# Kernel optimization log

Measured on AMD Instinct MI355X. Metric: run time of the kernel, lower is better.

The kernel has to match this reference:

```python
import jax, jax.numpy as jnp
import numpy as np

B, SQ, SV = 2, 2048, 2048
DV, DQ, DK, DO, H = 1024, 1280, 1024, 1024, 16
DHK, DHO = DK // H, DO // H


def setup_inputs() -> dict:
    key = jax.random.key(0)
    ks = jax.random.split(key, 8)
    pre_value_key = jax.random.normal(ks[0], (B, SV, DV), jnp.float32)
    pre_query = jax.random.normal(ks[1], (B, SQ, DQ), jnp.float32)
    value_key_masks = (jax.random.uniform(ks[2], (B, SV)) < 0.9).astype(jnp.float32)
    value_key_counts = jnp.maximum(value_key_masks.sum(-1), 1.0)
    s = 0.02
    Wq = jax.random.normal(ks[3], (DQ, DK), jnp.float32) * s
    bq = jnp.zeros((DK,), jnp.float32)
    Wk = jax.random.normal(ks[4], (DV, DK), jnp.float32) * s
    bk = jnp.zeros((DK,), jnp.float32)
    Wv = jax.random.normal(ks[5], (DV, DO), jnp.float32) * s
    bv = jnp.zeros((DO,), jnp.float32)
    overall_gain = jnp.ones((1, H, 1, 1), jnp.float32)
    overall_bias = jnp.full((1, H, 1, 1), -10.0, jnp.float32)
    return dict(pre_value_key=pre_value_key, pre_query=pre_query,
                value_key_masks=value_key_masks, value_key_counts=value_key_counts,
                Wq=Wq, bq=bq, Wk=Wk, bk=bk, Wv=Wv, bv=bv,
                overall_gain=overall_gain, overall_bias=overall_bias)


def _heads(x, h):
    # (B, S, D) -> (B, h, S, D//h)
    b, s, d = x.shape
    return x.reshape(b, s, h, d // h).transpose(0, 2, 1, 3)


def reference(pre_value_key, pre_query, value_key_masks, value_key_counts,
              Wq, bq, Wk, bk, Wv, bv, overall_gain, overall_bias):
    q = _heads(pre_query @ Wq + bq, H)        # (B,H,SQ,DHK)
    k = _heads(pre_value_key @ Wk + bk, H)    # (B,H,SV,DHK)
    v = _heads(pre_value_key @ Wv + bv, H)    # (B,H,SV,DHO)

    scores = jnp.einsum('bhqd,bhkd->bhqk', q, k) / jnp.sqrt(jnp.float32(DHK))

    mask = value_key_masks  # (B,SV), 0/1 float
    # pooled-score sigmoid gate (cross-attn branch)
    pooled = (scores * mask[:, None, None, :]).sum(-1, keepdims=True)
    pooled = pooled / value_key_counts[:, None, None, None]
    overall_weight = jax.nn.sigmoid(pooled * overall_gain + overall_bias)  # (B,H,SQ,1)

    add_mask = jnp.where(mask == 0, -jnp.inf, 0.0).astype(scores.dtype)
    sm = jax.nn.softmax(scores + add_mask[:, None, None, :], axis=-1)
    h = jnp.einsum('bhqk,bhkd->bhqd', sm, v)  # (B,H,SQ,DHO)

    pq_split = _heads(pre_query[:, :, :DO], H)  # (B,H,SQ,DHO)
    out = pq_split * (1.0 - overall_weight) + h * overall_weight
    out = out.transpose(0, 2, 1, 3).reshape(B, SQ, DO)
    out = jnp.concatenate([out, pre_query[:, :, DO:]], axis=-1)  # (B,SQ,DQ)
    return out
```

## Files before the change

kernel.cpp:

```cpp
#include <hip/hip_runtime.h>

typedef __attribute__((ext_vector_type(8))) __bf16 bf16x8;
typedef __attribute__((ext_vector_type(4))) float f32x4;
typedef __attribute__((ext_vector_type(16))) float f32x16;
typedef __attribute__((ext_vector_type(4))) unsigned short us4;
typedef __attribute__((ext_vector_type(4))) unsigned int u32x4;
typedef __attribute__((address_space(3))) void* as3vp;
typedef const __attribute__((address_space(1))) void* as1vp;

#define GLOAD_LDS16(g, l) __builtin_amdgcn_global_load_lds((as1vp)(g), (as3vp)(l), 16, 0, 0)

#if __has_builtin(__builtin_amdgcn_exp2f)
#define EXP2(x) __builtin_amdgcn_exp2f(x)
#else
#define EXP2(x) __expf((x) * 0.6931471805599453f)
#endif

__device__ __forceinline__ unsigned short f2bf(float f) {
  unsigned u = __builtin_bit_cast(unsigned, f);
  u += 0x7FFFu + ((u >> 16) & 1u);
  return (unsigned short)(u >> 16);
}
__device__ __forceinline__ float bf2f(unsigned short u) {
  return __builtin_bit_cast(float, (unsigned)u << 16);
}
__device__ __forceinline__ unsigned int pkbf(float a, float b) {
  unsigned int r;
  asm("v_cvt_pk_bf16_f32 %0, %1, %2" : "=v"(r) : "v"(a), "v"(b));
  return r;
}

__global__ void prep_all(const float* __restrict__ pre_q, const float* __restrict__ pre_vk,
                         const float* __restrict__ Wq, const float* __restrict__ Wk,
                         const float* __restrict__ Wv,
                         unsigned short* __restrict__ pq_bf, unsigned short* __restrict__ pv_bf,
                         unsigned short* __restrict__ WqT, unsigned short* __restrict__ WkT,
                         unsigned short* __restrict__ WvT, float* __restrict__ out) {
  __shared__ float tsh[32][33];
  const int bid = blockIdx.x, tid = threadIdx.x;
  if (bid < 5120) {
    const int i = bid * 256 + tid;
    float4 v = ((const float4*)pre_q)[i];
    us4 o;
    o.x = f2bf(v.x); o.y = f2bf(v.y); o.z = f2bf(v.z); o.w = f2bf(v.w);
    ((us4*)pq_bf)[i] = o;
    if ((i % 320) >= 256) ((float4*)out)[i] = v;
  } else if (bid < 9216) {
    const int i = (bid - 5120) * 256 + tid;
    float4 v = ((const float4*)pre_vk)[i];
    us4 o;
    o.x = f2bf(v.x); o.y = f2bf(v.y); o.z = f2bf(v.z); o.w = f2bf(v.w);
    ((us4*)pv_bf)[i] = o;
  } else {
    const int tb = bid - 9216;
    const int z = tb / 1280, rem = tb % 1280;
    const int x = rem & 31, y = rem >> 5;
    const int K = (z == 0) ? 1280 : 1024;
    if (y * 32 >= K) return;
    const float* W = (z == 0) ? Wq : ((z == 1) ? Wk : Wv);
    unsigned short* WT = (z == 0) ? WqT : ((z == 1) ? WkT : WvT);
    const int tx = tid & 31, ty = tid >> 5;
    const int n0 = x * 32, k0 = y * 32;
#pragma unroll
    for (int i = 0; i < 32; i += 8)
      tsh[ty + i][tx] = W[(size_t)(k0 + ty + i) * 1024 + n0 + tx];
    __syncthreads();
#pragma unroll
    for (int i = 0; i < 32; i += 8)
      WT[(size_t)(n0 + ty + i) * K + k0 + tx] = f2bf(tsh[tx][ty + i]);
  }
}

__global__ void km_reduce(const unsigned short* __restrict__ Kbb, const float* __restrict__ mask,
                          float* __restrict__ km, float* __restrict__ addm) {
  if (blockIdx.x < 16) {
    const int i = blockIdx.x * 256 + threadIdx.x;
    addm[i] = (mask[i] != 0.f) ? 0.f : -1e30f;
  }
  __shared__ float red[16][64];
  const int bh = blockIdx.x >> 3, chunk = blockIdx.x & 7;
  const int b = bh >> 4;
  const int dg = (threadIdx.x & 15) * 4, rg = threadIdx.x >> 4;
  const unsigned short* kb = Kbb + (size_t)(b * 2048) * 1024 + (bh & 15) * 64 + dg;
  const float* mr = mask + b * 2048;
  float a0 = 0.f, a1 = 0.f, a2 = 0.f, a3 = 0.f;
  const int kv0 = chunk * 256;
#pragma unroll 4
  for (int kv = kv0 + rg; kv < kv0 + 256; kv += 16) {
    const float mv = mr[kv];
    us4 kq = *(const us4*)(kb + (size_t)kv * 1024);
    a0 = fmaf(mv, bf2f(kq.x), a0); a1 = fmaf(mv, bf2f(kq.y), a1);
    a2 = fmaf(mv, bf2f(kq.z), a2); a3 = fmaf(mv, bf2f(kq.w), a3);
  }
  red[rg][dg] = a0; red[rg][dg + 1] = a1; red[rg][dg + 2] = a2; red[rg][dg + 3] = a3;
  __syncthreads();
  if (threadIdx.x < 64) {
    float s = 0.f;
#pragma unroll
    for (int i = 0; i < 16; ++i) s += red[i][threadIdx.x];
    atomicAdd(&km[bh * 64 + threadIdx.x], s);
  }
}

__global__ __launch_bounds__(256, 3)
void gemm_all(const unsigned short* __restrict__ Aq,
              const unsigned short* __restrict__ Akv,
              const unsigned short* __restrict__ WqT,
              const unsigned short* __restrict__ WkT,
              const unsigned short* __restrict__ WvT,
              const float* __restrict__ bq,
              const float* __restrict__ bk,
              const float* __restrict__ bv,
              unsigned short* __restrict__ Qout,
              unsigned short* __restrict__ Kout,
              unsigned short* __restrict__ VFout) {
  __shared__ unsigned short sAB[2][2][128 * 32];
  const int z = blockIdx.z;
  const int KDIM = (z == 0) ? 1280 : 1024;
  const unsigned short* A = (z == 0) ? Aq : Akv;
  const unsigned short* Bt = (z == 0) ? WqT : ((z == 1) ? WkT : WvT);

  const int tid = threadIdx.x, lane = tid & 63, w = tid >> 6;
  const int l15 = lane & 15, lhi = lane >> 4;
  const int wm = w >> 1, wn = w & 1;
  const int row0 = blockIdx.x * 128, col0 = blockIdx.y * 128;

  const f32x4 zv = {0.f, 0.f, 0.f, 0.f};
  f32x4 acc[4][4];
#pragma unroll
  for (int m = 0; m < 4; ++m)
#pragma unroll
    for (int n = 0; n < 4; ++n) acc[m][n] = zv;

  auto stage = [&](int buf, int kt) {
#pragma unroll
    for (int i = 0; i < 2; ++i) {
      const int c = i * 256 + tid;
      const int r = c >> 2, kc = ((c & 3) ^ (r & 3)) * 8;
      GLOAD_LDS16(A + (size_t)(row0 + r) * KDIM + kt + kc, &sAB[buf][0][0] + c * 8);
      GLOAD_LDS16(Bt + (size_t)(col0 + r) * KDIM + kt + kc, &sAB[buf][1][0] + c * 8);
    }
  };

  const int NT = KDIM / 32;
  stage(0, 0);
  __syncthreads();
  int cur = 0;
  for (int t = 0; t < NT; ++t) {
    if (t + 1 < NT) stage(cur ^ 1, (t + 1) * 32);
    const unsigned short* sAb = &sAB[cur][0][0];
    const unsigned short* sBb = &sAB[cur][1][0];
    const int koS = ((lhi ^ (l15 & 3)) * 8);
    bf16x8 af[4], bfr[4];
#pragma unroll
    for (int m = 0; m < 4; ++m) af[m] = *(const bf16x8*)(sAb + (wm * 64 + m * 16 + l15) * 32 + koS);
#pragma unroll
    for (int n = 0; n < 4; ++n) bfr[n] = *(const bf16x8*)(sBb + (wn * 64 + n * 16 + l15) * 32 + koS);
#pragma unroll
    for (int m = 0; m < 4; ++m)
#pragma unroll
      for (int n = 0; n < 4; ++n)
        acc[m][n] = __builtin_amdgcn_mfma_f32_16x16x32_bf16(af[m], bfr[n], acc[m][n], 0, 0, 0);
    __syncthreads();
    cur ^= 1;
  }

  if (z <= 1) {
    unsigned short* C = (z == 0) ? Qout : Kout;
    const float* bias = (z == 0) ? bq : bk;
    const float scale = (z == 0) ? 0.18033688f : 1.0f;
#pragma unroll
    for (int n = 0; n < 4; ++n) {
      const int gc = col0 + wn * 64 + n * 16 + l15;
      const float bb = bias[gc];
#pragma unroll
      for (int m = 0; m < 4; ++m) {
        const int gr0 = row0 + wm * 64 + m * 16 + lhi * 4;
#pragma unroll
        for (int r = 0; r < 4; ++r)
          C[(size_t)(gr0 + r) * 1024 + gc] = f2bf((acc[m][n][r] + bb) * scale);
      }
    }
  } else {
    __syncthreads();
    unsigned* tb = (unsigned*)&sAB[0][0][0];
#pragma unroll
    for (int n = 0; n < 4; ++n) {
      const int gcL = wn * 64 + n * 16 + l15;
      const float bb = bv[col0 + gcL];
#pragma unroll
      for (int m = 0; m < 4; ++m) {
#pragma unroll
        for (int k = 0; k < 2; ++k) {
          const int grPair = wm * 32 + m * 8 + lhi * 2 + k;
          const int W = (grPair & 3) | ((((grPair >> 2) ^ gcL) & 15) << 2);
          tb[gcL * 64 + W] = pkbf(acc[m][n][2 * k] + bb, acc[m][n][2 * k + 1] + bb);
        }
      }
    }
    __syncthreads();
    const int b_ = row0 >> 11;
#pragma unroll
    for (int it = 0; it < 8; ++it) {
      const int c = it * 256 + tid;
      const int gcL = (c & 63) + ((c >> 10) << 6);
      const int u = (c >> 6) & 15;
      const int W4 = (u ^ gcL) & 15;
      u32x4 o = *(const u32x4*)(tb + gcL * 64 + W4 * 4);
      const int kv0 = (row0 & 2047) + u * 8;
      const int ch = col0 + gcL;
      const int hh2 = ch >> 6, d = ch & 63;
      const int t2 = kv0 >> 6, ks2 = (kv0 >> 4) & 3, h5v = (kv0 >> 3) & 1;
      const size_t off = ((size_t)(b_ * 16 + hh2) << 17) +
                         (size_t)(((t2 * 4 + ks2) * 2 + (d >> 5)) * 64 + h5v * 32 + (d & 31)) * 8;
      *(u32x4*)(VFout + off) = o;
    }
  }
}

__global__ __launch_bounds__(256, 2)
void attn_fused(const unsigned short* __restrict__ Q,
                const unsigned short* __restrict__ Kb,
                const unsigned short* __restrict__ VF,
                const float* __restrict__ addm_g,
                const float* __restrict__ km,
                const float* __restrict__ counts,
                const float* __restrict__ gain,
                const float* __restrict__ gbias,
                const float* __restrict__ pq,
                float* __restrict__ out) {
  __shared__ __align__(16) char smem[32768];
  unsigned short* sK = (unsigned short*)smem;
  float* saddm = (float*)(smem + 16384);
  float* sOT = (float*)smem;

  const int tid = threadIdx.x, lane = tid & 63, w = tid >> 6;
  const int l31 = lane & 31, h5 = lane >> 5;
  const int f = blockIdx.x;
  const int qt = (f >> 3) & 15;
  const int bh = (f & 7) + 8 * (f >> 7);
  const int b = bh >> 4, hh = bh & 15;
  const int q0 = qt * 128;

  GLOAD_LDS16(addm_g + b * 2048 + tid * 4, (char*)saddm + tid * 16);
  GLOAD_LDS16(addm_g + b * 2048 + 1024 + tid * 4, (char*)saddm + 4096 + tid * 16);

  bf16x8 qf[4];
  {
    const unsigned short* qp = Q + (size_t)(b * 2048 + q0 + w * 32 + l31) * 1024 + hh * 64 + h5 * 8;
#pragma unroll
    for (int ks = 0; ks < 4; ++ks) qf[ks] = *(const bf16x8*)(qp + ks * 16);
  }

  float pl_s = 0.f;
  {
    const float* kmp = km + (b * 16 + hh) * 64 + h5 * 8;
#pragma unroll
    for (int ks = 0; ks < 4; ++ks) {
      f32x4 ka = *(const f32x4*)(kmp + ks * 16);
      f32x4 kb4 = *(const f32x4*)(kmp + ks * 16 + 4);
#pragma unroll
      for (int j = 0; j < 4; ++j)
        pl_s += (float)qf[ks][j] * ka[j] + (float)qf[ks][j + 4] * kb4[j];
    }
    float ta = pl_s, tb = pl_s;
    asm("v_permlane32_swap_b32 %0, %1" : "+v"(ta), "+v"(tb));
    pl_s = ta + tb;
  }

  const unsigned short* Kbase = Kb + (size_t)(b * 2048) * 1024 + hh * 64;
  const unsigned short* VFb = VF + ((size_t)bh << 17) + lane * 8;

  f32x16 o0, o1, l_vec;
#pragma unroll
  for (int r = 0; r < 16; ++r) { o0[r] = 0.f; o1[r] = 0.f; l_vec[r] = 0.f; }
  float m_ = -1e30f;

  auto stageK = [&](int buf, int kv) {
#pragma unroll
    for (int i = 0; i < 2; ++i) {
      const int c = i * 256 + tid;
      const int r = c >> 3, sl = (c & 7) ^ (r & 7);
      GLOAD_LDS16(Kbase + (size_t)(kv + r) * 1024 + sl * 8, (char*)sK + buf * 8192 + c * 16);
    }
  };

  bf16x8 vf[8];
  auto ldV = [&](int t) {
    const unsigned short* p = VFb + (size_t)t * 4096;
#pragma unroll
    for (int i = 0; i < 8; ++i) vf[i] = *(const bf16x8*)(p + i * 512);
  };

  stageK(0, 0);
  __syncthreads();
  int cur = 0;

  for (int t = 0; t < 32; ++t) {
    if (t < 31) stageK(cur ^ 1, (t + 1) * 64);
    ldV(t);
    const char* sKc = (const char*)sK + cur * 8192;

    f32x16 s0, s1;
#pragma unroll
    for (int g = 0; g < 4; ++g) {
      f32x4 a0 = *(const f32x4*)(saddm + t * 64 + g * 8 + h5 * 4);
      f32x4 a1 = *(const f32x4*)(saddm + t * 64 + 32 + g * 8 + h5 * 4);
#pragma unroll
      for (int j = 0; j < 4; ++j) { s0[g * 4 + j] = a0[j]; s1[g * 4 + j] = a1[j]; }
    }

#pragma unroll
    for (int ks = 0; ks < 4; ++ks) {
      const int sl = (((ks * 2 + h5) ^ (l31 & 7)) * 16);
      bf16x8 k0 = *(const bf16x8*)(sKc + l31 * 128 + sl);
      bf16x8 k1 = *(const bf16x8*)(sKc + (32 + l31) * 128 + sl);
      s0 = __builtin_amdgcn_mfma_f32_32x32x16_bf16(k0, qf[ks], s0, 0, 0, 0);
      s1 = __builtin_amdgcn_mfma_f32_32x32x16_bf16(k1, qf[ks], s1, 0, 0, 0);
    }

    f32x16 mx;
#pragma unroll
    for (int r = 0; r < 16; ++r) mx[r] = fmaxf(s0[r], s1[r]);
    float t8[8];
#pragma unroll
    for (int r = 0; r < 8; ++r) t8[r] = fmaxf(mx[r], mx[r + 8]);
    float tp = fmaxf(fmaxf(fmaxf(t8[0], t8[1]), fmaxf(t8[2], t8[3])),
                     fmaxf(fmaxf(t8[4], t8[5]), fmaxf(t8[6], t8[7])));
    {
      float ta = tp, tb = tp;
      asm("v_permlane32_swap_b32 %0, %1" : "+v"(ta), "+v"(tb));
      tp = fmaxf(ta, tb);
    }
    if (__any(tp > m_ + 11.0f)) {
      const float mnew = fmaxf(m_, tp);
      const float corr = EXP2(m_ - mnew);
      m_ = mnew;
      l_vec *= corr; o0 *= corr; o1 *= corr;
    }

    f32x16 p0, p1;
#pragma unroll
    for (int r = 0; r < 16; ++r) p0[r] = EXP2(s0[r] - m_);
#pragma unroll
    for (int r = 0; r < 16; ++r) p1[r] = EXP2(s1[r] - m_);
    l_vec += p0; l_vec += p1;

    bf16x8 pfs[4];
    {
      unsigned x0 = pkbf(p0[0], p0[1]), y0 = pkbf(p0[2], p0[3]);
      unsigned z0 = pkbf(p0[4], p0[5]), w0 = pkbf(p0[6], p0[7]);
      asm("v_permlane32_swap_b32 %0, %1" : "+v"(x0), "+v"(z0));
      asm("v_permlane32_swap_b32 %0, %1" : "+v"(y0), "+v"(w0));
      u32x4 f0 = {x0, y0, z0, w0};
      pfs[0] = __builtin_bit_cast(bf16x8, f0);
      unsigned x1 = pkbf(p0[8], p0[9]), y1 = pkbf(p0[10], p0[11]);
      unsigned z1 = pkbf(p0[12], p0[13]), w1 = pkbf(p0[14], p0[15]);
      asm("v_permlane32_swap_b32 %0, %1" : "+v"(x1), "+v"(z1));
      asm("v_permlane32_swap_b32 %0, %1" : "+v"(y1), "+v"(w1));
      u32x4 f1 = {x1, y1, z1, w1};
      pfs[1] = __builtin_bit_cast(bf16x8, f1);
      unsigned x2 = pkbf(p1[0], p1[1]), y2 = pkbf(p1[2], p1[3]);
      unsigned z2 = pkbf(p1[4], p1[5]), w2 = pkbf(p1[6], p1[7]);
      asm("v_permlane32_swap_b32 %0, %1" : "+v"(x2), "+v"(z2));
      asm("v_permlane32_swap_b32 %0, %1" : "+v"(y2), "+v"(w2));
      u32x4 f2 = {x2, y2, z2, w2};
      pfs[2] = __builtin_bit_cast(bf16x8, f2);
      unsigned x3 = pkbf(p1[8], p1[9]), y3 = pkbf(p1[10], p1[11]);
      unsigned z3 = pkbf(p1[12], p1[13]), w3 = pkbf(p1[14], p1[15]);
      asm("v_permlane32_swap_b32 %0, %1" : "+v"(x3), "+v"(z3));
      asm("v_permlane32_swap_b32 %0, %1" : "+v"(y3), "+v"(w3));
      u32x4 f3 = {x3, y3, z3, w3};
      pfs[3] = __builtin_bit_cast(bf16x8, f3);
    }

#pragma unroll
    for (int ks = 0; ks < 4; ++ks) {
      o0 = __builtin_amdgcn_mfma_f32_32x32x16_bf16(vf[ks * 2], pfs[ks], o0, 0, 0, 0);
      o1 = __builtin_amdgcn_mfma_f32_32x32x16_bf16(vf[ks * 2 + 1], pfs[ks], o1, 0, 0, 0);
    }
    __syncthreads();
    cur ^= 1;
  }

  float l_s;
  {
    float a[8];
#pragma unroll
    for (int r = 0; r < 8; ++r) a[r] = l_vec[r] + l_vec[r + 8];
    l_s = ((a[0] + a[1]) + (a[2] + a[3])) + ((a[4] + a[5]) + (a[6] + a[7]));
    float ta = l_s, tb = l_s;
    asm("v_permlane32_swap_b32 %0, %1" : "+v"(ta), "+v"(tb));
    l_s = ta + tb;
  }
  const float po = pl_s * 0.6931471805599453f / counts[b];
  const float wgv = 1.f / (1.f + __expf(-(po * gain[hh] + gbias[hh])));
  const float invl = 1.f / l_s;

  __syncthreads();
  float* myOT = sOT + w * 2048;
#pragma unroll
  for (int r = 0; r < 16; ++r) {
    const int d0 = (r & 3) + 8 * (r >> 2) + 4 * h5;
    myOT[d0 * 32 + (l31 ^ (d0 & 31))] = o0[r] * invl;
    const int d1 = d0 + 32;
    myOT[d1 * 32 + (l31 ^ (d1 & 31))] = o1[r] * invl;
  }
  __syncthreads();
  const size_t rowbase = (size_t)(b * 2048 + q0 + w * 32) * 1280 + hh * 64 + lane;
  const float* pqrow = pq + rowbase;
  float* outrow = out + rowbase;
#pragma unroll 4
  for (int i = 0; i < 32; ++i) {
    const float hval = myOT[lane * 32 + (i ^ (lane & 31))];
    const float wgrow = __shfl(wgv, i, 64);
    const float pv = pqrow[(size_t)i * 1280];
    outrow[(size_t)i * 1280] = fmaf(hval - pv, wgrow, pv);
  }
}

extern "C" void kernel_launch(void* const* d_in, const int* in_sizes, int n_in,
                              void* d_out, int out_size, void* d_ws, size_t ws_size,
                              hipStream_t stream) {
  const float* pre_vk = (const float*)d_in[0];
  const float* pre_q  = (const float*)d_in[1];
  const float* vmask  = (const float*)d_in[2];
  const float* vcnt   = (const float*)d_in[3];
  const float* Wq = (const float*)d_in[4];
  const float* bq = (const float*)d_in[5];
  const float* Wk = (const float*)d_in[6];
  const float* bk = (const float*)d_in[7];
  const float* Wv = (const float*)d_in[8];
  const float* bv = (const float*)d_in[9];
  const float* gain  = (const float*)d_in[10];
  const float* gbias = (const float*)d_in[11];
  float* out = (float*)d_out;

  char* ws = (char*)d_ws;
  unsigned short* pq_bf = (unsigned short*)(ws);
  unsigned short* pv_bf = (unsigned short*)(ws + 10485760);
  unsigned short* WqT   = (unsigned short*)(ws + 18874368);
  unsigned short* WkT   = (unsigned short*)(ws + 21495808);
  unsigned short* WvT   = (unsigned short*)(ws + 23592960);
  unsigned short* Qb    = (unsigned short*)(ws + 25690112);
  unsigned short* Kbb   = (unsigned short*)(ws + 34078720);
  unsigned short* VFb   = (unsigned short*)(ws + 42467328);
  float*          kmb   = (float*)(ws + 50855936);
  float*          addm  = (float*)(ws + 50864128);

  hipMemsetAsync(kmb, 0, 2 * 16 * 64 * sizeof(float), stream);
  prep_all<<<13056, 256, 0, stream>>>(pre_q, pre_vk, Wq, Wk, Wv,
                                      pq_bf, pv_bf, WqT, WkT, WvT, out);
  gemm_all<<<dim3(32, 8, 3), 256, 0, stream>>>(pq_bf, pv_bf, WqT, WkT, WvT, bq, bk, bv, Qb, Kbb, VFb);
  km_reduce<<<256, 256, 0, stream>>>(Kbb, vmask, kmb, addm);
  attn_fused<<<512, 256, 0, stream>>>(Qb, Kbb, VFb, addm, kmb, vcnt, gain, gbias, pre_q, out);
}
```

Baseline: 115.0 us.

## Fuse masked key-sum reduction into K projection epilogue and drop km_reduce

Removes the separate km_reduce kernel. The masked column sum of K is computed in the K-GEMM epilogue using shuffles and atomics, and the additive-mask build moves into extra blocks of prep_all. The GEMM grid is flattened to 1D with interleaved Q/K/V blocks so the three projections mix across CUs. This saves one launch and a re-read of K from memory, at the cost of more atomics and a slightly heavier epilogue.

```diff
diff --git a/kernel.cpp b/kernel.cpp
--- a/kernel.cpp
+++ b/kernel.cpp
@@ -32,10 +32,11 @@
 
 __global__ void prep_all(const float* __restrict__ pre_q, const float* __restrict__ pre_vk,
                          const float* __restrict__ Wq, const float* __restrict__ Wk,
-                         const float* __restrict__ Wv,
+                         const float* __restrict__ Wv, const float* __restrict__ vmask,
                          unsigned short* __restrict__ pq_bf, unsigned short* __restrict__ pv_bf,
                          unsigned short* __restrict__ WqT, unsigned short* __restrict__ WkT,
-                         unsigned short* __restrict__ WvT, float* __restrict__ out) {
+                         unsigned short* __restrict__ WvT, float* __restrict__ addm,
+                         float* __restrict__ out) {
   __shared__ float tsh[32][33];
   const int bid = blockIdx.x, tid = threadIdx.x;
   if (bid < 5120) {
@@ -51,7 +52,7 @@
     us4 o;
     o.x = f2bf(v.x); o.y = f2bf(v.y); o.z = f2bf(v.z); o.w = f2bf(v.w);
     ((us4*)pv_bf)[i] = o;
-  } else {
+  } else if (bid < 13056) {
     const int tb = bid - 9216;
     const int z = tb / 1280, rem = tb % 1280;
     const int x = rem & 31, y = rem >> 5;
@@ -68,37 +69,9 @@
 #pragma unroll
     for (int i = 0; i < 32; i += 8)
       WT[(size_t)(n0 + ty + i) * K + k0 + tx] = f2bf(tsh[tx][ty + i]);
-  }
-}
-
-__global__ void km_reduce(const unsigned short* __restrict__ Kbb, const float* __restrict__ mask,
-                          float* __restrict__ km, float* __restrict__ addm) {
-  if (blockIdx.x < 16) {
-    const int i = blockIdx.x * 256 + threadIdx.x;
-    addm[i] = (mask[i] != 0.f) ? 0.f : -1e30f;
-  }
-  __shared__ float red[16][64];
-  const int bh = blockIdx.x >> 3, chunk = blockIdx.x & 7;
-  const int b = bh >> 4;
-  const int dg = (threadIdx.x & 15) * 4, rg = threadIdx.x >> 4;
-  const unsigned short* kb = Kbb + (size_t)(b * 2048) * 1024 + (bh & 15) * 64 + dg;
-  const float* mr = mask + b * 2048;
-  float a0 = 0.f, a1 = 0.f, a2 = 0.f, a3 = 0.f;
-  const int kv0 = chunk * 256;
-#pragma unroll 4
-  for (int kv = kv0 + rg; kv < kv0 + 256; kv += 16) {
-    const float mv = mr[kv];
-    us4 kq = *(const us4*)(kb + (size_t)kv * 1024);
-    a0 = fmaf(mv, bf2f(kq.x), a0); a1 = fmaf(mv, bf2f(kq.y), a1);
-    a2 = fmaf(mv, bf2f(kq.z), a2); a3 = fmaf(mv, bf2f(kq.w), a3);
-  }
-  red[rg][dg] = a0; red[rg][dg + 1] = a1; red[rg][dg + 2] = a2; red[rg][dg + 3] = a3;
-  __syncthreads();
-  if (threadIdx.x < 64) {
-    float s = 0.f;
-#pragma unroll
-    for (int i = 0; i < 16; ++i) s += red[i][threadIdx.x];
-    atomicAdd(&km[bh * 64 + threadIdx.x], s);
+  } else {
+    const int i = (bid - 13056) * 256 + tid;
+    addm[i] = (vmask[i] != 0.f) ? 0.f : -1e30f;
   }
 }
 
@@ -111,11 +84,16 @@
               const float* __restrict__ bq,
               const float* __restrict__ bk,
               const float* __restrict__ bv,
+              const float* __restrict__ vmask,
               unsigned short* __restrict__ Qout,
               unsigned short* __restrict__ Kout,
-              unsigned short* __restrict__ VFout) {
+              unsigned short* __restrict__ VFout,
+              float* __restrict__ km) {
   __shared__ unsigned short sAB[2][2][128 * 32];
-  const int z = blockIdx.z;
+  const int fblk = blockIdx.x;
+  const int z = fblk % 3;
+  const int rest = fblk / 3;
+  const int bx = rest & 31, by = rest >> 5;
   const int KDIM = (z == 0) ? 1280 : 1024;
   const unsigned short* A = (z == 0) ? Aq : Akv;
   const unsigned short* Bt = (z == 0) ? WqT : ((z == 1) ? WkT : WvT);
@@ -123,7 +101,7 @@
   const int tid = threadIdx.x, lane = tid & 63, w = tid >> 6;
   const int l15 = lane & 15, lhi = lane >> 4;
   const int wm = w >> 1, wn = w & 1;
-  const int row0 = blockIdx.x * 128, col0 = blockIdx.y * 128;
+  const int row0 = bx * 128, col0 = by * 128;
 
   const f32x4 zv = {0.f, 0.f, 0.f, 0.f};
   f32x4 acc[4][4];
@@ -165,21 +143,44 @@
     cur ^= 1;
   }
 
-  if (z <= 1) {
-    unsigned short* C = (z == 0) ? Qout : Kout;
-    const float* bias = (z == 0) ? bq : bk;
-    const float scale = (z == 0) ? 0.18033688f : 1.0f;
+  if (z == 0) {
 #pragma unroll
     for (int n = 0; n < 4; ++n) {
       const int gc = col0 + wn * 64 + n * 16 + l15;
-      const float bb = bias[gc];
+      const float bb = bq[gc];
 #pragma unroll
       for (int m = 0; m < 4; ++m) {
         const int gr0 = row0 + wm * 64 + m * 16 + lhi * 4;
 #pragma unroll
         for (int r = 0; r < 4; ++r)
-          C[(size_t)(gr0 + r) * 1024 + gc] = f2bf((acc[m][n][r] + bb) * scale);
+          Qout[(size_t)(gr0 + r) * 1024 + gc] = f2bf((acc[m][n][r] + bb) * 0.18033688f);
       }
+    }
+  } else if (z == 1) {
+    const int b_ = row0 >> 11;
+    const float* maskb = vmask + b_ * 2048;
+    f32x4 mv[4];
+#pragma unroll
+    for (int m = 0; m < 4; ++m)
+      mv[m] = *(const f32x4*)(maskb + (row0 & 2047) + wm * 64 + m * 16 + lhi * 4);
+#pragma unroll
+    for (int n = 0; n < 4; ++n) {
+      const int gc = col0 + wn * 64 + n * 16 + l15;
+      const float bb = bk[gc];
+      float s = 0.f;
+#pragma unroll
+      for (int m = 0; m < 4; ++m) {
+        const int gr0 = row0 + wm * 64 + m * 16 + lhi * 4;
+#pragma unroll
+        for (int r = 0; r < 4; ++r) {
+          const float val = acc[m][n][r] + bb;
+          Kout[(size_t)(gr0 + r) * 1024 + gc] = f2bf(val);
+          s = fmaf(mv[m][r], val, s);
+        }
+      }
+      s += __shfl_xor(s, 16, 64);
+      s += __shfl_xor(s, 32, 64);
+      if (lhi == 0) atomicAdd(&km[(b_ * 16 + (gc >> 6)) * 64 + (gc & 63)], s);
     }
   } else {
     __syncthreads();
@@ -449,9 +450,9 @@
   float*          addm  = (float*)(ws + 50864128);
 
   hipMemsetAsync(kmb, 0, 2 * 16 * 64 * sizeof(float), stream);
-  prep_all<<<13056, 256, 0, stream>>>(pre_q, pre_vk, Wq, Wk, Wv,
-                                      pq_bf, pv_bf, WqT, WkT, WvT, out);
-  gemm_all<<<dim3(32, 8, 3), 256, 0, stream>>>(pq_bf, pv_bf, WqT, WkT, WvT, bq, bk, bv, Qb, Kbb, VFb);
-  km_reduce<<<256, 256, 0, stream>>>(Kbb, vmask, kmb, addm);
+  prep_all<<<13072, 256, 0, stream>>>(pre_q, pre_vk, Wq, Wk, Wv, vmask,
+                                      pq_bf, pv_bf, WqT, WkT, WvT, addm, out);
+  gemm_all<<<768, 256, 0, stream>>>(pq_bf, pv_bf, WqT, WkT, WvT, bq, bk, bv, vmask,
+                                    Qb, Kbb, VFb, kmb);
   attn_fused<<<512, 256, 0, stream>>>(Qb, Kbb, VFb, addm, kmb, vcnt, gain, gbias, pre_q, out);
 }
```

New measurement: 111.8 us. 2.8% less time.
